# Kernel tuning notes

Measured on AMD Instinct MI355X. Metric: run time of the kernel, lower is better.

The kernel has to match this reference:

```python
import jax, jax.numpy as jnp
import numpy as np
from jax import lax

B, N, S, K = 16, 4096, 1024, 32
RADIUS = 0.2
C_IN = 64
BN_EPS = 1e-5


def setup_inputs() -> dict:
    key = jax.random.key(0)
    ks = jax.random.split(key, 6)
    x = jax.random.normal(ks[0], (B, N, 3), dtype=jnp.float32)
    x_complete = jax.random.normal(ks[1], (B, N, C_IN), dtype=jnp.float32)
    W0 = jax.random.normal(ks[2], (64, 67), dtype=jnp.float32) * 0.1
    W1 = jax.random.normal(ks[3], (64, 64), dtype=jnp.float32) * 0.1
    W2 = jax.random.normal(ks[4], (128, 64), dtype=jnp.float32) * 0.1
    return {
        "x": x, "x_complete": x_complete,
        "W0": W0, "b0": jnp.zeros(64), "g0": jnp.ones(64), "be0": jnp.zeros(64),
        "W1": W1, "b1": jnp.zeros(64), "g1": jnp.ones(64), "be1": jnp.zeros(64),
        "W2": W2, "b2": jnp.zeros(128), "g2": jnp.ones(128), "be2": jnp.zeros(128),
    }


def _fps(xyz, n_samples):
    """Farthest point sampling. xyz: [B,N,3] -> indices [B,n_samples] (int32)."""
    b, n, _ = xyz.shape
    batch_ar = jnp.arange(b)

    def step(carry, _):
        dists, farthest = carry                      # [B,N], [B]
        centroid = xyz[batch_ar, farthest]           # [B,3]
        d = jnp.sum((xyz - centroid[:, None, :]) ** 2, axis=-1)  # [B,N]
        dists = jnp.minimum(dists, d)
        nxt = jnp.argmax(dists, axis=-1).astype(jnp.int32)
        return (dists, nxt), farthest

    init = (jnp.full((b, n), 1e10, dtype=xyz.dtype), jnp.zeros(b, dtype=jnp.int32))
    _, idx = lax.scan(step, init, None, length=n_samples)
    return idx.T                                     # [B,n_samples]


def _ball_query(xyz, new_xyz, radius, k):
    """First-k points within radius of each centroid. Returns [B,S,K] int32."""
    b, n, _ = xyz.shape
    # squared distances centroid->point: [B,S,N]
    d2 = jnp.sum((new_xyz[:, :, None, :] - xyz[:, None, :, :]) ** 2, axis=-1)
    idx = jnp.where(d2 <= radius * radius, jnp.arange(n, dtype=jnp.int32), jnp.int32(n))
    idx = jnp.sort(idx, axis=-1)[..., :k]            # first k in index order
    first = idx[..., :1]                             # centroid itself is always in ball
    idx = jnp.where(idx == n, first, idx)
    return jnp.minimum(idx, n - 1)


def _gather_points(pts, idx_flat):
    """pts [B,N,C], idx_flat [B,M] -> [B,M,C]."""
    return jnp.take_along_axis(pts, idx_flat[..., None], axis=1)


def _conv_bn_relu(f, W, b, g, be):
    """f [B,C,M]; 1x1 Conv1d + training-mode BatchNorm1d + ReLU."""
    y = jnp.einsum('bcm,dc->bdm', f, W) + b[None, :, None]
    mu = jnp.mean(y, axis=(0, 2), keepdims=True)
    var = jnp.var(y, axis=(0, 2), keepdims=True)
    y = (y - mu) * lax.rsqrt(var + BN_EPS) * g[None, :, None] + be[None, :, None]
    return jax.nn.relu(y)


def reference(x, x_complete, W0, b0, g0, be0, W1, b1, g1, be1, W2, b2, g2, be2):
    # 1) FPS sampling of S centroids
    fps_idx = _fps(x, S)                                     # [B,S]
    new_xyz = _gather_points(x, fps_idx)                     # [B,S,3]
    # 2) Ball-query grouping of K neighbors per centroid
    idx = _ball_query(x, new_xyz, RADIUS, K)                 # [B,S,K]
    idx_flat = idx.reshape(B, S * K)
    grouped_xyz = _gather_points(x, idx_flat).reshape(B, S, K, 3)
    grouped_xyz = grouped_xyz - new_xyz[:, :, None, :]       # relative coords
    grouped_feat = _gather_points(x_complete, idx_flat).reshape(B, S, K, C_IN)
    f = jnp.concatenate([grouped_xyz, grouped_feat], axis=-1)  # [B,S,K,67]
    # 3) Shared MLP over channel dim (Conv1d k=1 + BN + ReLU), channels-first
    f = f.reshape(B, S * K, 3 + C_IN).transpose(0, 2, 1)     # [B,67,S*K]
    f = _conv_bn_relu(f, W0, b0, g0, be0)
    f = _conv_bn_relu(f, W1, b1, g1, be1)
    f = _conv_bn_relu(f, W2, b2, g2, be2)                    # [B,128,S*K]
    # 4) Max-pool over the K neighbors per centroid
    out = jnp.max(f.reshape(B, 128, S, K), axis=3)           # [B,128,S]
    return out
```

## Files before the change

### kernel.cpp

```cpp
#include <hip/hip_runtime.h>

namespace {
constexpr int kB = 16;
constexpr int kN = 4096;
constexpr int kS = 1024;
constexpr int kK = 32;
constexpr int kCF = 67;
constexpr int kSK = kS * kK;
constexpr int kPT = kB * kSK;
constexpr float kM = 524288.0f;

constexpr size_t kOffIdx   = 196608;
constexpr size_t kOffStats = 2293760;
constexpr size_t kOffScsh  = 2295808;
constexpr size_t kOffU     = 2297856;
constexpr size_t kWsNeedU  = kOffU + (size_t)kB * kN * 64 * sizeof(float);
constexpr size_t kOffPmax  = 19075072;
constexpr size_t kOffPmin  = kOffPmax + 8388608;
constexpr size_t kOffY1    = kOffPmin + 8388608;
constexpr size_t kWsNeedF  = kOffY1 + (size_t)kPT * 64 * 2;

constexpr int kLdsK = 72;

using bf16x8 = __attribute__((ext_vector_type(8))) short;
using f32x4  = __attribute__((ext_vector_type(4))) float;
}

__device__ __forceinline__ unsigned short f2bf(float f) {
  unsigned u = __float_as_uint(f);
  u += 0x7fffu + ((u >> 16) & 1u);
  return (unsigned short)(u >> 16);
}
__device__ __forceinline__ unsigned pack2bf(float a, float b) {
  return (unsigned)f2bf(a) | ((unsigned)f2bf(b) << 16);
}

template <int CTRL, int RM>
__device__ __forceinline__ float fmax_dpp(float x) {
  const int m = __builtin_amdgcn_update_dpp(__float_as_int(x), __float_as_int(x),
                                            CTRL, RM, 0xf, false);
  return fmaxf(x, __int_as_float(m));
}
template <int CTRL, int RM>
__device__ __forceinline__ unsigned umin_dpp(unsigned x) {
  const unsigned m = (unsigned)__builtin_amdgcn_update_dpp((int)x, (int)x,
                                                           CTRL, RM, 0xf, false);
  return x < m ? x : m;
}

__device__ void fps_body(const float* __restrict__ x, float* __restrict__ new_xyz,
                         int b, int tid, char* smem) {
  float* xs = (float*)smem;
  float* ys = xs + kN;
  float* zs = ys + kN;
  float* pv = zs + kN;
  int*   pi = (int*)(pv + 8);
  const int lane = tid & 63;
  const int wid = tid >> 6;
  const float* xb = x + (size_t)b * kN * 3;
  for (int q = tid; q < kN; q += 256) {
    xs[q] = xb[q * 3 + 0];
    ys[q] = xb[q * 3 + 1];
    zs[q] = xb[q * 3 + 2];
  }
  __syncthreads();
  float px[16], py[16], pz[16], dm[16];
#pragma unroll
  for (int j = 0; j < 16; ++j) {
    const int p = tid * 16 + j;
    px[j] = xs[p]; py[j] = ys[p]; pz[j] = zs[p];
    dm[j] = 1e10f;
  }
  int far = 0;
  for (int i = 0; i < kS; ++i) {
    const float cx = xs[far], cy = ys[far], cz = zs[far];
    if (tid == 0) {
      float* o = new_xyz + ((size_t)b * kS + i) * 3;
      o[0] = cx; o[1] = cy; o[2] = cz;
    }
#pragma unroll
    for (int j = 0; j < 16; ++j) {
      const float dx = __fsub_rn(px[j], cx);
      const float dy = __fsub_rn(py[j], cy);
      const float dz = __fsub_rn(pz[j], cz);
      const float t = __fadd_rn(__fadd_rn(__fmul_rn(dx, dx), __fmul_rn(dy, dy)),
                                __fmul_rn(dz, dz));
      dm[j] = fminf(dm[j], t);
    }
    const float m0 = fmaxf(fmaxf(dm[0], dm[1]), dm[2]);
    const float m1 = fmaxf(fmaxf(dm[3], dm[4]), dm[5]);
    const float m2 = fmaxf(fmaxf(dm[6], dm[7]), dm[8]);
    const float m3 = fmaxf(fmaxf(dm[9], dm[10]), dm[11]);
    const float m4 = fmaxf(fmaxf(dm[12], dm[13]), dm[14]);
    const float n0 = fmaxf(fmaxf(m0, m1), dm[15]);
    const float n1 = fmaxf(fmaxf(m2, m3), m4);
    float v = fmaxf(n0, n1);
    v = fmax_dpp<0x111, 0xf>(v);
    v = fmax_dpp<0x112, 0xf>(v);
    v = fmax_dpp<0x114, 0xf>(v);
    v = fmax_dpp<0x118, 0xf>(v);
    v = fmax_dpp<0x142, 0xa>(v);
    v = fmax_dpp<0x143, 0xc>(v);
    const float wv = __int_as_float(__builtin_amdgcn_readlane(__float_as_int(v), 63));
    unsigned msk = 0;
#pragma unroll
    for (int j = 0; j < 16; ++j) msk |= (dm[j] == wv ? 1u : 0u) << j;
    unsigned cand = msk ? ((unsigned)(tid * 16) + (unsigned)__builtin_ctz(msk))
                        : 0xffffffffu;
    cand = umin_dpp<0x111, 0xf>(cand);
    cand = umin_dpp<0x112, 0xf>(cand);
    cand = umin_dpp<0x114, 0xf>(cand);
    cand = umin_dpp<0x118, 0xf>(cand);
    cand = umin_dpp<0x142, 0xa>(cand);
    cand = umin_dpp<0x143, 0xc>(cand);
    const unsigned widx = (unsigned)__builtin_amdgcn_readlane((int)cand, 63);
    const int par = i & 1;
    if (lane == 0) { pv[par * 4 + wid] = wv; pi[par * 4 + wid] = (int)widx; }
    __syncthreads();
    float fv = pv[par * 4 + 0];
    int fi = pi[par * 4 + 0];
#pragma unroll
    for (int w = 1; w < 4; ++w) {
      const float v2 = pv[par * 4 + w];
      const int i2 = pi[par * 4 + w];
      if (v2 > fv) { fv = v2; fi = i2; }
    }
    far = fi;
  }
}

__device__ void u_body(const float* __restrict__ xc, const float* __restrict__ W0,
                       float* __restrict__ U, int ublk, int tid, char* smem) {
  unsigned short* a_lds = (unsigned short*)smem;
  unsigned short* w_lds = (unsigned short*)(smem + 128 * kLdsK * 2);
  const int r0 = ublk * 128;
  {
    const int pt = tid >> 1, half = tid & 1;
    const float4* src = (const float4*)(xc + ((size_t)(r0 + pt)) * 64 + half * 32);
    unsigned* dst = (unsigned*)(a_lds + pt * kLdsK + half * 32);
#pragma unroll
    for (int i = 0; i < 8; ++i) {
      const float4 v = src[i];
      dst[2 * i + 0] = pack2bf(v.x, v.y);
      dst[2 * i + 1] = pack2bf(v.z, v.w);
    }
  }
  for (int e = tid; e < 64 * 64; e += 256) {
    const int d = e >> 6, k2 = e & 63;
    w_lds[d * kLdsK + k2] = f2bf(W0[d * kCF + 3 + k2]);
  }
  __syncthreads();
  const int w = tid >> 6, lane = tid & 63, lr = lane & 15, lk = lane >> 4;
  f32x4 acc[2][4];
#pragma unroll
  for (int mi = 0; mi < 2; ++mi)
#pragma unroll
    for (int ni = 0; ni < 4; ++ni) acc[mi][ni] = (f32x4){0.f, 0.f, 0.f, 0.f};
#pragma unroll
  for (int ks = 0; ks < 2; ++ks) {
    const int k = lk * 8 + ks * 32;
    const bf16x8 a0 = *(const bf16x8*)(a_lds + (32 * w + lr) * kLdsK + k);
    const bf16x8 a1 = *(const bf16x8*)(a_lds + (32 * w + 16 + lr) * kLdsK + k);
#pragma unroll
    for (int ni = 0; ni < 4; ++ni) {
      const bf16x8 bv = *(const bf16x8*)(w_lds + (16 * ni + lr) * kLdsK + k);
      acc[0][ni] = __builtin_amdgcn_mfma_f32_16x16x32_bf16(a0, bv, acc[0][ni], 0, 0, 0);
      acc[1][ni] = __builtin_amdgcn_mfma_f32_16x16x32_bf16(a1, bv, acc[1][ni], 0, 0, 0);
    }
  }
#pragma unroll
  for (int mi = 0; mi < 2; ++mi)
#pragma unroll
    for (int ni = 0; ni < 4; ++ni)
#pragma unroll
      for (int r = 0; r < 4; ++r) {
        const int row = 32 * w + 16 * mi + lk * 4 + r;
        U[((size_t)(r0 + row)) * 64 + 16 * ni + lr] = acc[mi][ni][r];
      }
}

__global__ __launch_bounds__(256) void k1_kernel(const float* __restrict__ x,
                                                 const float* __restrict__ xc,
                                                 const float* __restrict__ W0,
                                                 float* __restrict__ nxyz,
                                                 float* __restrict__ U) {
  __shared__ __align__(16) char smem[49664];
  if (blockIdx.x < 16) fps_body(x, nxyz, blockIdx.x, threadIdx.x, smem);
  else u_body(xc, W0, U, blockIdx.x - 16, threadIdx.x, smem);
}

__global__ __launch_bounds__(256) void ballq_kernel(const float* __restrict__ x,
                                                    const float* __restrict__ new_xyz,
                                                    int* __restrict__ idx) {
  const int g = blockIdx.x * 4 + (threadIdx.x >> 6);
  const int lane = threadIdx.x & 63;
  const int b = g >> 10;
  const float* xb = x + (size_t)b * kN * 3;
  const float nx = new_xyz[g * 3 + 0];
  const float ny = new_xyz[g * 3 + 1];
  const float nz = new_xyz[g * 3 + 2];
  const float RR = (float)(0.2 * 0.2);
  int cnt = 0;
  int first = -1;
  for (int c = 0; c < kN / 64 && cnt < kK; ++c) {
    const int p = c * 64 + lane;
    const float dx = __fsub_rn(xb[p * 3 + 0], nx);
    const float dy = __fsub_rn(xb[p * 3 + 1], ny);
    const float dz = __fsub_rn(xb[p * 3 + 2], nz);
    const float t = __fadd_rn(__fadd_rn(__fmul_rn(dx, dx), __fmul_rn(dy, dy)),
                              __fmul_rn(dz, dz));
    const bool within = (t <= RR);
    const unsigned long long m = __ballot(within);
    if (first < 0 && m != 0ull) first = c * 64 + __builtin_ctzll(m);
    const int pos = cnt + (int)__popcll(m & ((1ull << lane) - 1ull));
    if (within && pos < kK) idx[(size_t)g * kK + pos] = p;
    cnt += (int)__popcll(m);
  }
  for (int k2 = cnt + lane; k2 < kK; k2 += 64) idx[(size_t)g * kK + k2] = first;
}

__global__ __launch_bounds__(256) void stats0_kernel(
    const float* __restrict__ x, const float* __restrict__ nxyz,
    const int* __restrict__ idx, const float* __restrict__ U,
    const float* __restrict__ W0, const float* __restrict__ b0,
    float* __restrict__ stats) {
  __shared__ float4 w0c[64];
  __shared__ float red[128];
  const int tid = threadIdx.x;
  if (tid < 64) w0c[tid] = make_float4(W0[tid * kCF + 0], W0[tid * kCF + 1],
                                       W0[tid * kCF + 2], b0[tid]);
  if (tid < 128) red[tid] = 0.0f;
  __syncthreads();
  const int gid = blockIdx.x * 256 + tid;
  const int half = gid & 1;
  const int pbase = gid >> 1;
  float s[32], q[32];
#pragma unroll
  for (int i = 0; i < 32; ++i) { s[i] = 0.f; q[i] = 0.f; }
  for (int r = 0; r < 8; ++r) {
    const int pt = pbase + r * 65536;
    const int v = idx[pt];
    const int b = pt >> 15;
    const int sc = (pt & (kSK - 1)) >> 5;
    const float* xp = x + ((size_t)b * kN + v) * 3;
    const float* np = nxyz + ((size_t)b * kS + sc) * 3;
    const float rx = xp[0] - np[0], ry = xp[1] - np[1], rz = xp[2] - np[2];
    const float4* up = (const float4*)(U + ((size_t)b * kN + v) * 64 + half * 32);
#pragma unroll
    for (int i = 0; i < 8; ++i) {
      const float4 u4 = up[i];
      const float uu[4] = {u4.x, u4.y, u4.z, u4.w};
#pragma unroll
      for (int j = 0; j < 4; ++j) {
        const float4 wc = w0c[half * 32 + i * 4 + j];
        const float y = uu[j] + rx * wc.x + ry * wc.y + rz * wc.z + wc.w;
        s[i * 4 + j] += y;
        q[i * 4 + j] += y * y;
      }
    }
  }
#pragma unroll
  for (int i = 0; i < 32; ++i) {
    const int c = half * 32 + i;
    atomicAdd(&red[c], s[i]);
    atomicAdd(&red[64 + c], q[i]);
  }
  __syncthreads();
  if (tid < 128) atomicAdd(&stats[tid], red[tid]);
}

__global__ void finalize_kernel(const float* __restrict__ g, const float* __restrict__ be,
                                const float* __restrict__ st, float* __restrict__ sc,
                                float* __restrict__ sh, int C) {
  const int c = threadIdx.x;
  if (c < C) {
    const float mean = st[c] / kM;
    const float var = st[C + c] / kM - mean * mean;
    const float scale = g[c] / sqrtf(var + 1e-5f);
    sc[c] = scale;
    sh[c] = be[c] - mean * scale;
  }
}

__global__ __launch_bounds__(256) void mlpA_kernel(
    const float* __restrict__ x, const float* __restrict__ nxyz,
    const int* __restrict__ idx, const float* __restrict__ U,
    const float* __restrict__ W0, const float* __restrict__ b0,
    const float* __restrict__ W1, const float* __restrict__ b1v,
    const float* __restrict__ scsh, float* __restrict__ stats,
    unsigned short* __restrict__ y1out) {
  __shared__ unsigned short a_lds[128 * kLdsK];
  __shared__ unsigned short w_lds[64 * kLdsK];
  __shared__ float red[128];
  __shared__ float4 w0c[64];
  __shared__ float2 sc0l[64];
  const int tid = threadIdx.x;
  const int p0 = blockIdx.x * 128;
  if (tid < 128) red[tid] = 0.0f;
  if (tid < 64) {
    w0c[tid] = make_float4(W0[tid * kCF + 0], W0[tid * kCF + 1],
                           W0[tid * kCF + 2], b0[tid]);
    sc0l[tid] = make_float2(scsh[tid], scsh[64 + tid]);
  }
  for (int f = tid; f < 64 * 16; f += 256) {
    const int d = f >> 4, k4 = (f & 15) * 4;
    const float4 vw = *(const float4*)(W1 + d * 64 + k4);
    unsigned* dst = (unsigned*)(w_lds + d * kLdsK + k4);
    dst[0] = pack2bf(vw.x, vw.y);
    dst[1] = pack2bf(vw.z, vw.w);
  }
  __syncthreads();
  {
    const int pt = tid >> 1, half = tid & 1;
    const int pg = p0 + pt;
    const int v = idx[pg];
    const int b = pg >> 15;
    const int sct = (pg & (kSK - 1)) >> 5;
    const float* xp = x + ((size_t)b * kN + v) * 3;
    const float* np = nxyz + ((size_t)b * kS + sct) * 3;
    const float rx = xp[0] - np[0], ry = xp[1] - np[1], rz = xp[2] - np[2];
    const float4* up = (const float4*)(U + ((size_t)b * kN + v) * 64 + half * 32);
    unsigned* dst = (unsigned*)(a_lds + pt * kLdsK + half * 32);
#pragma unroll
    for (int i = 0; i < 8; ++i) {
      const float4 u4 = up[i];
      const float uu[4] = {u4.x, u4.y, u4.z, u4.w};
      float a1[4];
#pragma unroll
      for (int j = 0; j < 4; ++j) {
        const int c = half * 32 + i * 4 + j;
        const float4 wc = w0c[c];
        const float y = uu[j] + rx * wc.x + ry * wc.y + rz * wc.z + wc.w;
        const float2 ss = sc0l[c];
        a1[j] = fmaxf(fmaf(y, ss.x, ss.y), 0.0f);
      }
      dst[2 * i + 0] = pack2bf(a1[0], a1[1]);
      dst[2 * i + 1] = pack2bf(a1[2], a1[3]);
    }
  }
  __syncthreads();

  const int w = tid >> 6, lane = tid & 63, lr = lane & 15, lk = lane >> 4;
  f32x4 acc1[2][4];
#pragma unroll
  for (int mi = 0; mi < 2; ++mi)
#pragma unroll
    for (int ni = 0; ni < 4; ++ni) acc1[mi][ni] = (f32x4){0.f, 0.f, 0.f, 0.f};
#pragma unroll
  for (int ks = 0; ks < 2; ++ks) {
    const int k = lk * 8 + ks * 32;
    const bf16x8 a0 = *(const bf16x8*)(a_lds + (32 * w + lr) * kLdsK + k);
    const bf16x8 a1 = *(const bf16x8*)(a_lds + (32 * w + 16 + lr) * kLdsK + k);
#pragma unroll
    for (int ni = 0; ni < 4; ++ni) {
      const bf16x8 bv = *(const bf16x8*)(w_lds + (16 * ni + lr) * kLdsK + k);
      acc1[0][ni] = __builtin_amdgcn_mfma_f32_16x16x32_bf16(a0, bv, acc1[0][ni], 0, 0, 0);
      acc1[1][ni] = __builtin_amdgcn_mfma_f32_16x16x32_bf16(a1, bv, acc1[1][ni], 0, 0, 0);
    }
  }
#pragma unroll
  for (int ni = 0; ni < 4; ++ni) {
    const int ch = 16 * ni + lr;
    const float bb = b1v[ch];
    float ss = 0.f, qq = 0.f;
#pragma unroll
    for (int mi = 0; mi < 2; ++mi)
#pragma unroll
      for (int r = 0; r < 4; ++r) {
        const float y = acc1[mi][ni][r] + bb;
        ss += y;
        qq += y * y;
        const int row = 32 * w + 16 * mi + lk * 4 + r;
        a_lds[row * kLdsK + ch] = f2bf(y);
      }
    atomicAdd(&red[ch], ss);
    atomicAdd(&red[64 + ch], qq);
  }
  __syncthreads();
  {
    const int row = tid >> 1, hf = tid & 1;
    const uint4* s4 = (const uint4*)(a_lds + row * kLdsK + hf * 32);
    uint4* d4 = (uint4*)(y1out + (size_t)(p0 + row) * 64 + hf * 32);
    d4[0] = s4[0]; d4[1] = s4[1]; d4[2] = s4[2]; d4[3] = s4[3];
  }
  if (tid < 128) atomicAdd(&stats[128 + tid], red[tid]);
}

__global__ __launch_bounds__(256) void mlpB_kernel(
    const unsigned short* __restrict__ y1in, const float* __restrict__ W2,
    const float* __restrict__ b2v, const float* __restrict__ scsh,
    float* __restrict__ stats, float* __restrict__ pmax,
    float* __restrict__ pmin) {
  __shared__ unsigned short a_lds[128 * kLdsK];
  __shared__ unsigned short w_lds[128 * kLdsK];
  __shared__ float red[256];
  __shared__ float2 s1l[64];
  const int tid = threadIdx.x;
  const int p0 = blockIdx.x * 128;
  red[tid] = 0.0f;
  if (tid < 64) s1l[tid] = make_float2(scsh[128 + tid], scsh[192 + tid]);
  __syncthreads();
  for (int f = tid; f < 128 * 16; f += 256) {
    const int d = f >> 4, k4 = (f & 15) * 4;
    const float4 vw = *(const float4*)(W2 + d * 64 + k4);
    unsigned* dst = (unsigned*)(w_lds + d * kLdsK + k4);
    dst[0] = pack2bf(vw.x, vw.y);
    dst[1] = pack2bf(vw.z, vw.w);
  }
  {
    const int row = tid >> 1, hf = tid & 1;
    const uint4* src = (const uint4*)(y1in + (size_t)(p0 + row) * 64 + hf * 32);
    const uint4 qa = src[0], qb = src[1], qc = src[2], qd = src[3];
    const unsigned in[16] = {qa.x, qa.y, qa.z, qa.w, qb.x, qb.y, qb.z, qb.w,
                             qc.x, qc.y, qc.z, qc.w, qd.x, qd.y, qd.z, qd.w};
    unsigned* dst = (unsigned*)(a_lds + row * kLdsK) + hf * 16;
#pragma unroll
    for (int i2 = 0; i2 < 16; ++i2) {
      const unsigned u = in[i2];
      const int ch0 = hf * 32 + i2 * 2;
      const float2 sA = s1l[ch0];
      const float2 sB = s1l[ch0 + 1];
      const float flo = __uint_as_float(u << 16);
      const float fhi = __uint_as_float(u & 0xffff0000u);
      const float alo = fmaxf(fmaf(flo, sA.x, sA.y), 0.0f);
      const float ahi = fmaxf(fmaf(fhi, sB.x, sB.y), 0.0f);
      dst[i2] = pack2bf(alo, ahi);
    }
  }
  __syncthreads();

  const int w = tid >> 6, lane = tid & 63, lr = lane & 15, lk = lane >> 4;
  f32x4 acc2[2][8];
#pragma unroll
  for (int mi = 0; mi < 2; ++mi)
#pragma unroll
    for (int ni = 0; ni < 8; ++ni) acc2[mi][ni] = (f32x4){0.f, 0.f, 0.f, 0.f};
#pragma unroll
  for (int ks = 0; ks < 2; ++ks) {
    const int k = lk * 8 + ks * 32;
    const bf16x8 a0 = *(const bf16x8*)(a_lds + (32 * w + lr) * kLdsK + k);
    const bf16x8 a1 = *(const bf16x8*)(a_lds + (32 * w + 16 + lr) * kLdsK + k);
#pragma unroll
    for (int ni = 0; ni < 8; ++ni) {
      const bf16x8 bv = *(const bf16x8*)(w_lds + (16 * ni + lr) * kLdsK + k);
      acc2[0][ni] = __builtin_amdgcn_mfma_f32_16x16x32_bf16(a0, bv, acc2[0][ni], 0, 0, 0);
      acc2[1][ni] = __builtin_amdgcn_mfma_f32_16x16x32_bf16(a1, bv, acc2[1][ni], 0, 0, 0);
    }
  }
  float mxv[8], mnv[8];
#pragma unroll
  for (int ni = 0; ni < 8; ++ni) {
    const int ch = 16 * ni + lr;
    const float bb = b2v[ch];
    float ss = 0.f, qq = 0.f;
    float mx = -3.4e38f, mn = 3.4e38f;
#pragma unroll
    for (int mi = 0; mi < 2; ++mi)
#pragma unroll
      for (int r = 0; r < 4; ++r) {
        const float a = acc2[mi][ni][r];
        const float y = a + bb;
        ss += y;
        qq += y * y;
        mx = fmaxf(mx, a);
        mn = fminf(mn, a);
      }
    atomicAdd(&red[ch], ss);
    atomicAdd(&red[128 + ch], qq);
    mx = fmaxf(mx, __shfl_xor(mx, 16, 64));
    mx = fmaxf(mx, __shfl_xor(mx, 32, 64));
    mn = fminf(mn, __shfl_xor(mn, 16, 64));
    mn = fminf(mn, __shfl_xor(mn, 32, 64));
    mxv[ni] = mx + bb;
    mnv[ni] = mn + bb;
  }
  __syncthreads();
  atomicAdd(&stats[256 + tid], red[tid]);
  const int pg0 = p0 + 32 * w;
  const int ob = pg0 >> 15;
  const int os = (pg0 & (kSK - 1)) >> 5;
  if (lane < 16) {
#pragma unroll
    for (int ni = 0; ni < 8; ++ni) {
      const size_t off = ((size_t)ob * 128 + 16 * ni + lane) * kS + os;
      pmax[off] = mxv[ni];
      pmin[off] = mnv[ni];
    }
  }
}

__global__ __launch_bounds__(256) void poolbn_kernel(
    const float* __restrict__ pmax, const float* __restrict__ pmin,
    const float* __restrict__ scsh, float* __restrict__ out) {
  const int gid = blockIdx.x * 256 + threadIdx.x;
  const int c = (gid >> 10) & 127;
  const float sc = scsh[256 + c];
  const float sh = scsh[384 + c];
  const float p = (sc >= 0.f) ? pmax[gid] : pmin[gid];
  out[gid] = fmaxf(fmaf(p, sc, sh), 0.0f);
}

template <int STAGE>
__global__ __launch_bounds__(256) void mlp_kernel(
    const float* __restrict__ x, const float* __restrict__ nxyz,
    const int* __restrict__ idx, const float* __restrict__ U,
    const float* __restrict__ W0, const float* __restrict__ b0,
    const float* __restrict__ W1, const float* __restrict__ b1v,
    const float* __restrict__ W2, const float* __restrict__ b2v,
    const float* __restrict__ scsh, float* __restrict__ stats,
    float* __restrict__ out) {
  __shared__ unsigned short a_lds[128 * kLdsK];
  __shared__ unsigned short w_lds[128 * kLdsK];
  __shared__ float red[256];
  __shared__ float4 w0c[64];
  __shared__ float2 sc0l[64];
  const int tid = threadIdx.x;
  const int p0 = blockIdx.x * 128;
  red[tid] = 0.0f;
  if (tid < 64) {
    w0c[tid] = make_float4(W0[tid * kCF + 0], W0[tid * kCF + 1],
                           W0[tid * kCF + 2], b0[tid]);
    sc0l[tid] = make_float2(scsh[tid], scsh[64 + tid]);
  }
  for (int f = tid; f < 64 * 16; f += 256) {
    const int d = f >> 4, k4 = (f & 15) * 4;
    const float4 vw = *(const float4*)(W1 + d * 64 + k4);
    unsigned* dst = (unsigned*)(w_lds + d * kLdsK + k4);
    dst[0] = pack2bf(vw.x, vw.y);
    dst[1] = pack2bf(vw.z, vw.w);
  }
  __syncthreads();
  {
    const int pt = tid >> 1, half = tid & 1;
    const int pg = p0 + pt;
    const int v = idx[pg];
    const int b = pg >> 15;
    const int sct = (pg & (kSK - 1)) >> 5;
    const float* xp = x + ((size_t)b * kN + v) * 3;
    const float* np = nxyz + ((size_t)b * kS + sct) * 3;
    const float rx = xp[0] - np[0], ry = xp[1] - np[1], rz = xp[2] - np[2];
    const float4* up = (const float4*)(U + ((size_t)b * kN + v) * 64 + half * 32);
    unsigned* dst = (unsigned*)(a_lds + pt * kLdsK + half * 32);
#pragma unroll
    for (int i = 0; i < 8; ++i) {
      const float4 u4 = up[i];
      const float uu[4] = {u4.x, u4.y, u4.z, u4.w};
      float a1[4];
#pragma unroll
      for (int j = 0; j < 4; ++j) {
        const int c = half * 32 + i * 4 + j;
        const float4 wc = w0c[c];
        const float y = uu[j] + rx * wc.x + ry * wc.y + rz * wc.z + wc.w;
        const float2 ss = sc0l[c];
        a1[j] = fmaxf(fmaf(y, ss.x, ss.y), 0.0f);
      }
      dst[2 * i + 0] = pack2bf(a1[0], a1[1]);
      dst[2 * i + 1] = pack2bf(a1[2], a1[3]);
    }
  }
  __syncthreads();

  const int w = tid >> 6, lane = tid & 63, lr = lane & 15, lk = lane >> 4;
  f32x4 acc1[2][4];
#pragma unroll
  for (int mi = 0; mi < 2; ++mi)
#pragma unroll
    for (int ni = 0; ni < 4; ++ni) acc1[mi][ni] = (f32x4){0.f, 0.f, 0.f, 0.f};
#pragma unroll
  for (int ks = 0; ks < 2; ++ks) {
    const int k = lk * 8 + ks * 32;
    const bf16x8 a0 = *(const bf16x8*)(a_lds + (32 * w + lr) * kLdsK + k);
    const bf16x8 a1 = *(const bf16x8*)(a_lds + (32 * w + 16 + lr) * kLdsK + k);
#pragma unroll
    for (int ni = 0; ni < 4; ++ni) {
      const bf16x8 bv = *(const bf16x8*)(w_lds + (16 * ni + lr) * kLdsK + k);
      acc1[0][ni] = __builtin_amdgcn_mfma_f32_16x16x32_bf16(a0, bv, acc1[0][ni], 0, 0, 0);
      acc1[1][ni] = __builtin_amdgcn_mfma_f32_16x16x32_bf16(a1, bv, acc1[1][ni], 0, 0, 0);
    }
  }

  if constexpr (STAGE == 1) {
#pragma unroll
    for (int ni = 0; ni < 4; ++ni) {
      const int ch = 16 * ni + lr;
      const float bb = b1v[ch];
      float ss = 0.f, qq = 0.f;
#pragma unroll
      for (int mi = 0; mi < 2; ++mi)
#pragma unroll
        for (int r = 0; r < 4; ++r) {
          const float y = acc1[mi][ni][r] + bb;
          ss += y;
          qq += y * y;
        }
      atomicAdd(&red[ch], ss);
      atomicAdd(&red[64 + ch], qq);
    }
    __syncthreads();
    if (tid < 128) atomicAdd(&stats[128 + tid], red[tid]);
    return;
  } else {
    __syncthreads();
#pragma unroll
    for (int ni = 0; ni < 4; ++ni) {
      const int ch = 16 * ni + lr;
      const float bb = b1v[ch];
      const float sc1 = scsh[128 + ch], sh1 = scsh[192 + ch];
#pragma unroll
      for (int mi = 0; mi < 2; ++mi)
#pragma unroll
        for (int r = 0; r < 4; ++r) {
          const int row = 32 * w + 16 * mi + lk * 4 + r;
          const float val = fmaxf(fmaf(acc1[mi][ni][r] + bb, sc1, sh1), 0.0f);
          a_lds[row * kLdsK + ch] = f2bf(val);
        }
    }
    for (int f = tid; f < 128 * 16; f += 256) {
      const int d = f >> 4, k4 = (f & 15) * 4;
      const float4 vw = *(const float4*)(W2 + d * 64 + k4);
      unsigned* dst = (unsigned*)(w_lds + d * kLdsK + k4);
      dst[0] = pack2bf(vw.x, vw.y);
      dst[1] = pack2bf(vw.z, vw.w);
    }
    __syncthreads();

    f32x4 acc2[2][8];
#pragma unroll
    for (int mi = 0; mi < 2; ++mi)
#pragma unroll
      for (int ni = 0; ni < 8; ++ni) acc2[mi][ni] = (f32x4){0.f, 0.f, 0.f, 0.f};
#pragma unroll
    for (int ks = 0; ks < 2; ++ks) {
      const int k = lk * 8 + ks * 32;
      const bf16x8 a0 = *(const bf16x8*)(a_lds + (32 * w + lr) * kLdsK + k);
      const bf16x8 a1 = *(const bf16x8*)(a_lds + (32 * w + 16 + lr) * kLdsK + k);
#pragma unroll
      for (int ni = 0; ni < 8; ++ni) {
        const bf16x8 bv = *(const bf16x8*)(w_lds + (16 * ni + lr) * kLdsK + k);
        acc2[0][ni] = __builtin_amdgcn_mfma_f32_16x16x32_bf16(a0, bv, acc2[0][ni], 0, 0, 0);
        acc2[1][ni] = __builtin_amdgcn_mfma_f32_16x16x32_bf16(a1, bv, acc2[1][ni], 0, 0, 0);
      }
    }

    if constexpr (STAGE == 2) {
#pragma unroll
      for (int ni = 0; ni < 8; ++ni) {
        const int ch = 16 * ni + lr;
        const float bb = b2v[ch];
        float ss = 0.f, qq = 0.f;
#pragma unroll
        for (int mi = 0; mi < 2; ++mi)
#pragma unroll
          for (int r = 0; r < 4; ++r) {
            const float y = acc2[mi][ni][r] + bb;
            ss += y;
            qq += y * y;
          }
        atomicAdd(&red[ch], ss);
        atomicAdd(&red[128 + ch], qq);
      }
      __syncthreads();
      atomicAdd(&stats[256 + tid], red[tid]);
    } else {
      float mx[8];
#pragma unroll
      for (int ni = 0; ni < 8; ++ni) {
        const int ch = 16 * ni + lr;
        const float bb = b2v[ch];
        const float sc2 = scsh[256 + ch], sh2 = scsh[384 + ch];
        float m = -1.0f;
#pragma unroll
        for (int mi = 0; mi < 2; ++mi)
#pragma unroll
          for (int r = 0; r < 4; ++r)
            m = fmaxf(m, fmaxf(fmaf(acc2[mi][ni][r] + bb, sc2, sh2), 0.0f));
        mx[ni] = m;
      }
#pragma unroll
      for (int ni = 0; ni < 8; ++ni) {
        mx[ni] = fmaxf(mx[ni], __shfl_xor(mx[ni], 16, 64));
        mx[ni] = fmaxf(mx[ni], __shfl_xor(mx[ni], 32, 64));
      }
      const int pg0 = p0 + 32 * w;
      const int ob = pg0 >> 15;
      const int os = (pg0 & (kSK - 1)) >> 5;
      if (lane < 16) {
#pragma unroll
        for (int ni = 0; ni < 8; ++ni)
          out[((size_t)ob * 128 + 16 * ni + lane) * kS + os] = mx[ni];
      }
    }
  }
}

extern "C" void kernel_launch(void* const* d_in, const int* in_sizes, int n_in,
                              void* d_out, int out_size, void* d_ws, size_t ws_size,
                              hipStream_t stream) {
  const float* x   = (const float*)d_in[0];
  const float* xc  = (const float*)d_in[1];
  const float* W0  = (const float*)d_in[2];
  const float* b0  = (const float*)d_in[3];
  const float* g0  = (const float*)d_in[4];
  const float* be0 = (const float*)d_in[5];
  const float* W1  = (const float*)d_in[6];
  const float* b1  = (const float*)d_in[7];
  const float* g1  = (const float*)d_in[8];
  const float* be1 = (const float*)d_in[9];
  const float* W2  = (const float*)d_in[10];
  const float* b2  = (const float*)d_in[11];
  const float* g2  = (const float*)d_in[12];
  const float* be2 = (const float*)d_in[13];
  float* out = (float*)d_out;
  char* ws = (char*)d_ws;
  float* nxyz  = (float*)(ws);
  int*   idx   = (int*)(ws + kOffIdx);
  float* stats = (float*)(ws + kOffStats);
  float* scsh  = (float*)(ws + kOffScsh);
  float* U     = (float*)(ws + kOffU);
  float* pmax  = (float*)(ws + kOffPmax);
  float* pmin  = (float*)(ws + kOffPmin);
  unsigned short* y1 = (unsigned short*)(ws + kOffY1);
  (void)in_sizes; (void)n_in; (void)out_size;

  hipMemsetAsync(stats, 0, 512 * sizeof(float), stream);
  k1_kernel<<<16 + 512, 256, 0, stream>>>(x, xc, W0, nxyz, U);
  ballq_kernel<<<(kB * kS) / 4, 256, 0, stream>>>(x, nxyz, idx);
  stats0_kernel<<<512, 256, 0, stream>>>(x, nxyz, idx, U, W0, b0, stats);
  finalize_kernel<<<1, 128, 0, stream>>>(g0, be0, stats, scsh, scsh + 64, 64);

  if (ws_size >= kWsNeedF) {
    mlpA_kernel<<<kPT / 128, 256, 0, stream>>>(x, nxyz, idx, U, W0, b0, W1, b1,
                                               scsh, stats, y1);
    finalize_kernel<<<1, 128, 0, stream>>>(g1, be1, stats + 128, scsh + 128, scsh + 192, 64);
    mlpB_kernel<<<kPT / 128, 256, 0, stream>>>(y1, W2, b2, scsh, stats, pmax, pmin);
    finalize_kernel<<<1, 128, 0, stream>>>(g2, be2, stats + 256, scsh + 256, scsh + 384, 128);
    poolbn_kernel<<<(kB * 128 * kS) / 256, 256, 0, stream>>>(pmax, pmin, scsh, out);
  } else {
    mlp_kernel<1><<<kPT / 128, 256, 0, stream>>>(x, nxyz, idx, U, W0, b0, W1, b1,
                                                 W2, b2, scsh, stats, out);
    finalize_kernel<<<1, 128, 0, stream>>>(g1, be1, stats + 128, scsh + 128, scsh + 192, 64);
    mlp_kernel<2><<<kPT / 128, 256, 0, stream>>>(x, nxyz, idx, U, W0, b0, W1, b1,
                                                 W2, b2, scsh, stats, out);
    finalize_kernel<<<1, 128, 0, stream>>>(g2, be2, stats + 256, scsh + 256, scsh + 384, 128);
    mlp_kernel<3><<<kPT / 128, 256, 0, stream>>>(x, nxyz, idx, U, W0, b0, W1, b1,
                                                 W2, b2, scsh, stats, out);
  }
}
```

Measured before the change: 1.187 ms.

## Overlap ball query and BN0 stats with FPS using in-kernel progress flags

Fuses the ball-query and layer-0 statistics kernels into the FPS/U kernel as persistent worker blocks. The workers spin on per-batch progress flags that FPS publishes every 16 centroids, plus a counter for U completion, so neighbour search overlaps the long serial FPS loop instead of waiting for it. The FPS argmax is also reworked to pack distance and inverted index into a 64-bit key, giving a single max reduction instead of a max pass followed by an index-min pass. The FPS blocks get raised wave priority. This relies on all blocks being co-resident, since spin-waiting blocks could deadlock if the producer blocks are not scheduled, and the sleeping waiters take CU slots alongside the FPS waves.

```diff
diff --git a/kernel.cpp b/kernel.cpp
--- a/kernel.cpp
+++ b/kernel.cpp
@@ -13,9 +13,9 @@
 constexpr size_t kOffIdx   = 196608;
 constexpr size_t kOffStats = 2293760;
 constexpr size_t kOffScsh  = 2295808;
-constexpr size_t kOffU     = 2297856;
-constexpr size_t kWsNeedU  = kOffU + (size_t)kB * kN * 64 * sizeof(float);
-constexpr size_t kOffPmax  = 19075072;
+constexpr size_t kOffFlags = 2297856;
+constexpr size_t kOffU     = 2297984;
+constexpr size_t kOffPmax  = kOffU + 16777216;
 constexpr size_t kOffPmin  = kOffPmax + 8388608;
 constexpr size_t kOffY1    = kOffPmin + 8388608;
 constexpr size_t kWsNeedF  = kOffY1 + (size_t)kPT * 64 * 2;
@@ -24,6 +24,7 @@
 
 using bf16x8 = __attribute__((ext_vector_type(8))) short;
 using f32x4  = __attribute__((ext_vector_type(4))) float;
+using u64 = unsigned long long;
 }
 
 __device__ __forceinline__ unsigned short f2bf(float f) {
@@ -35,26 +36,24 @@
   return (unsigned)f2bf(a) | ((unsigned)f2bf(b) << 16);
 }
 
+__device__ __forceinline__ u64 kmax(u64 a, u64 b) { return a > b ? a : b; }
+
 template <int CTRL, int RM>
-__device__ __forceinline__ float fmax_dpp(float x) {
-  const int m = __builtin_amdgcn_update_dpp(__float_as_int(x), __float_as_int(x),
-                                            CTRL, RM, 0xf, false);
-  return fmaxf(x, __int_as_float(m));
-}
-template <int CTRL, int RM>
-__device__ __forceinline__ unsigned umin_dpp(unsigned x) {
-  const unsigned m = (unsigned)__builtin_amdgcn_update_dpp((int)x, (int)x,
-                                                           CTRL, RM, 0xf, false);
-  return x < m ? x : m;
+__device__ __forceinline__ u64 kmax_dpp(u64 x) {
+  const unsigned hi = (unsigned)(x >> 32), lo = (unsigned)x;
+  const unsigned h2 = (unsigned)__builtin_amdgcn_update_dpp((int)hi, (int)hi, CTRL, RM, 0xf, false);
+  const unsigned l2 = (unsigned)__builtin_amdgcn_update_dpp((int)lo, (int)lo, CTRL, RM, 0xf, false);
+  const u64 y = ((u64)h2 << 32) | l2;
+  return x > y ? x : y;
 }
 
 __device__ void fps_body(const float* __restrict__ x, float* __restrict__ new_xyz,
-                         int b, int tid, char* smem) {
+                         int* __restrict__ flags, int b, int tid, char* smem) {
+  __builtin_amdgcn_s_setprio(3);
   float* xs = (float*)smem;
   float* ys = xs + kN;
   float* zs = ys + kN;
-  float* pv = zs + kN;
-  int*   pi = (int*)(pv + 8);
+  u64* pvu = (u64*)(smem + 49152);
   const int lane = tid & 63;
   const int wid = tid >> 6;
   const float* xb = x + (size_t)b * kN * 3;
@@ -65,11 +64,13 @@
   }
   __syncthreads();
   float px[16], py[16], pz[16], dm[16];
+  unsigned invc[16];
 #pragma unroll
   for (int j = 0; j < 16; ++j) {
     const int p = tid * 16 + j;
     px[j] = xs[p]; py[j] = ys[p]; pz[j] = zs[p];
     dm[j] = 1e10f;
+    invc[j] = 0xffffffffu - (unsigned)p;
   }
   int far = 0;
   for (int i = 0; i < kS; ++i) {
@@ -77,6 +78,9 @@
     if (tid == 0) {
       float* o = new_xyz + ((size_t)b * kS + i) * 3;
       o[0] = cx; o[1] = cy; o[2] = cz;
+      if ((i & 15) == 15)
+        __hip_atomic_store(&flags[b], i + 1, __ATOMIC_RELEASE,
+                           __HIP_MEMORY_SCOPE_AGENT);
     }
 #pragma unroll
     for (int j = 0; j < 16; ++j) {
@@ -87,50 +91,36 @@
                                 __fmul_rn(dz, dz));
       dm[j] = fminf(dm[j], t);
     }
-    const float m0 = fmaxf(fmaxf(dm[0], dm[1]), dm[2]);
-    const float m1 = fmaxf(fmaxf(dm[3], dm[4]), dm[5]);
-    const float m2 = fmaxf(fmaxf(dm[6], dm[7]), dm[8]);
-    const float m3 = fmaxf(fmaxf(dm[9], dm[10]), dm[11]);
-    const float m4 = fmaxf(fmaxf(dm[12], dm[13]), dm[14]);
-    const float n0 = fmaxf(fmaxf(m0, m1), dm[15]);
-    const float n1 = fmaxf(fmaxf(m2, m3), m4);
-    float v = fmaxf(n0, n1);
-    v = fmax_dpp<0x111, 0xf>(v);
-    v = fmax_dpp<0x112, 0xf>(v);
-    v = fmax_dpp<0x114, 0xf>(v);
-    v = fmax_dpp<0x118, 0xf>(v);
-    v = fmax_dpp<0x142, 0xa>(v);
-    v = fmax_dpp<0x143, 0xc>(v);
-    const float wv = __int_as_float(__builtin_amdgcn_readlane(__float_as_int(v), 63));
-    unsigned msk = 0;
-#pragma unroll
-    for (int j = 0; j < 16; ++j) msk |= (dm[j] == wv ? 1u : 0u) << j;
-    unsigned cand = msk ? ((unsigned)(tid * 16) + (unsigned)__builtin_ctz(msk))
-                        : 0xffffffffu;
-    cand = umin_dpp<0x111, 0xf>(cand);
-    cand = umin_dpp<0x112, 0xf>(cand);
-    cand = umin_dpp<0x114, 0xf>(cand);
-    cand = umin_dpp<0x118, 0xf>(cand);
-    cand = umin_dpp<0x142, 0xa>(cand);
-    cand = umin_dpp<0x143, 0xc>(cand);
-    const unsigned widx = (unsigned)__builtin_amdgcn_readlane((int)cand, 63);
+    u64 k[16];
+#pragma unroll
+    for (int j = 0; j < 16; ++j)
+      k[j] = ((u64)__float_as_uint(dm[j]) << 32) | invc[j];
+    u64 t8[8], t4[4], t2[2];
+#pragma unroll
+    for (int j = 0; j < 8; ++j) t8[j] = kmax(k[j], k[j + 8]);
+#pragma unroll
+    for (int j = 0; j < 4; ++j) t4[j] = kmax(t8[j], t8[j + 4]);
+#pragma unroll
+    for (int j = 0; j < 2; ++j) t2[j] = kmax(t4[j], t4[j + 2]);
+    u64 v = kmax(t2[0], t2[1]);
+    v = kmax_dpp<0x111, 0xf>(v);
+    v = kmax_dpp<0x112, 0xf>(v);
+    v = kmax_dpp<0x114, 0xf>(v);
+    v = kmax_dpp<0x118, 0xf>(v);
+    v = kmax_dpp<0x142, 0xa>(v);
+    v = kmax_dpp<0x143, 0xc>(v);
     const int par = i & 1;
-    if (lane == 0) { pv[par * 4 + wid] = wv; pi[par * 4 + wid] = (int)widx; }
+    if (lane == 63) pvu[par * 4 + wid] = v;
     __syncthreads();
-    float fv = pv[par * 4 + 0];
-    int fi = pi[par * 4 + 0];
-#pragma unroll
-    for (int w = 1; w < 4; ++w) {
-      const float v2 = pv[par * 4 + w];
-      const int i2 = pi[par * 4 + w];
-      if (v2 > fv) { fv = v2; fi = i2; }
-    }
-    far = fi;
+    const u64 mm = kmax(kmax(pvu[par * 4 + 0], pvu[par * 4 + 1]),
+                        kmax(pvu[par * 4 + 2], pvu[par * 4 + 3]));
+    far = (int)(0xffffffffu - (unsigned)mm);
   }
 }
 
 __device__ void u_body(const float* __restrict__ xc, const float* __restrict__ W0,
-                       float* __restrict__ U, int ublk, int tid, char* smem) {
+                       float* __restrict__ U, int* __restrict__ flags,
+                       int ublk, int tid, char* smem) {
   unsigned short* a_lds = (unsigned short*)smem;
   unsigned short* w_lds = (unsigned short*)(smem + 128 * kLdsK * 2);
   const int r0 = ublk * 128;
@@ -177,74 +167,68 @@
         const int row = 32 * w + 16 * mi + lk * 4 + r;
         U[((size_t)(r0 + row)) * 64 + 16 * ni + lr] = acc[mi][ni][r];
       }
-}
-
-__global__ __launch_bounds__(256) void k1_kernel(const float* __restrict__ x,
-                                                 const float* __restrict__ xc,
-                                                 const float* __restrict__ W0,
-                                                 float* __restrict__ nxyz,
-                                                 float* __restrict__ U) {
-  __shared__ __align__(16) char smem[49664];
-  if (blockIdx.x < 16) fps_body(x, nxyz, blockIdx.x, threadIdx.x, smem);
-  else u_body(xc, W0, U, blockIdx.x - 16, threadIdx.x, smem);
-}
-
-__global__ __launch_bounds__(256) void ballq_kernel(const float* __restrict__ x,
-                                                    const float* __restrict__ new_xyz,
-                                                    int* __restrict__ idx) {
-  const int g = blockIdx.x * 4 + (threadIdx.x >> 6);
-  const int lane = threadIdx.x & 63;
-  const int b = g >> 10;
-  const float* xb = x + (size_t)b * kN * 3;
-  const float nx = new_xyz[g * 3 + 0];
-  const float ny = new_xyz[g * 3 + 1];
-  const float nz = new_xyz[g * 3 + 2];
-  const float RR = (float)(0.2 * 0.2);
-  int cnt = 0;
-  int first = -1;
-  for (int c = 0; c < kN / 64 && cnt < kK; ++c) {
-    const int p = c * 64 + lane;
-    const float dx = __fsub_rn(xb[p * 3 + 0], nx);
-    const float dy = __fsub_rn(xb[p * 3 + 1], ny);
-    const float dz = __fsub_rn(xb[p * 3 + 2], nz);
-    const float t = __fadd_rn(__fadd_rn(__fmul_rn(dx, dx), __fmul_rn(dy, dy)),
-                              __fmul_rn(dz, dz));
-    const bool within = (t <= RR);
-    const unsigned long long m = __ballot(within);
-    if (first < 0 && m != 0ull) first = c * 64 + __builtin_ctzll(m);
-    const int pos = cnt + (int)__popcll(m & ((1ull << lane) - 1ull));
-    if (within && pos < kK) idx[(size_t)g * kK + pos] = p;
-    cnt += (int)__popcll(m);
-  }
-  for (int k2 = cnt + lane; k2 < kK; k2 += 64) idx[(size_t)g * kK + k2] = first;
-}
-
-__global__ __launch_bounds__(256) void stats0_kernel(
-    const float* __restrict__ x, const float* __restrict__ nxyz,
-    const int* __restrict__ idx, const float* __restrict__ U,
-    const float* __restrict__ W0, const float* __restrict__ b0,
-    float* __restrict__ stats) {
-  __shared__ float4 w0c[64];
-  __shared__ float red[128];
-  const int tid = threadIdx.x;
+  __syncthreads();
+  if (tid == 0)
+    __hip_atomic_fetch_add(&flags[16], 1, __ATOMIC_RELEASE,
+                           __HIP_MEMORY_SCOPE_AGENT);
+}
+
+__device__ void ballq_stats_body(const float* __restrict__ x,
+                                 const float* __restrict__ nxyz,
+                                 int* __restrict__ idx,
+                                 const float* __restrict__ U,
+                                 const float* __restrict__ W0,
+                                 const float* __restrict__ b0,
+                                 float* __restrict__ stats,
+                                 int* __restrict__ flags,
+                                 int blk, int tid, char* smem) {
+  float* red = (float*)smem;
+  float4* w0c = (float4*)(smem + 512);
+  if (tid < 128) red[tid] = 0.0f;
   if (tid < 64) w0c[tid] = make_float4(W0[tid * kCF + 0], W0[tid * kCF + 1],
                                        W0[tid * kCF + 2], b0[tid]);
-  if (tid < 128) red[tid] = 0.0f;
-  __syncthreads();
-  const int gid = blockIdx.x * 256 + tid;
-  const int half = gid & 1;
-  const int pbase = gid >> 1;
-  float s[32], q[32];
-#pragma unroll
-  for (int i = 0; i < 32; ++i) { s[i] = 0.f; q[i] = 0.f; }
-  for (int r = 0; r < 8; ++r) {
-    const int pt = pbase + r * 65536;
-    const int v = idx[pt];
-    const int b = pt >> 15;
-    const int sc = (pt & (kSK - 1)) >> 5;
+  __syncthreads();
+  const int wid = tid >> 6, lane = tid & 63;
+  const int W = blk * 4 + wid;
+  while (__hip_atomic_load(&flags[16], __ATOMIC_RELAXED,
+                           __HIP_MEMORY_SCOPE_AGENT) < 512)
+    __builtin_amdgcn_s_sleep(32);
+  (void)__hip_atomic_load(&flags[16], __ATOMIC_ACQUIRE, __HIP_MEMORY_SCOPE_AGENT);
+  const float RR = (float)(0.2 * 0.2);
+  const int half = lane & 1;
+  float s_acc[32], q_acc[32];
+#pragma unroll
+  for (int i = 0; i < 32; ++i) { s_acc[i] = 0.f; q_acc[i] = 0.f; }
+  for (int g = W; g < kB * kS; g += 896) {
+    const int b = g >> 10;
+    const int s = g & 1023;
+    while (__hip_atomic_load(&flags[b], __ATOMIC_RELAXED,
+                             __HIP_MEMORY_SCOPE_AGENT) <= s)
+      __builtin_amdgcn_s_sleep(32);
+    (void)__hip_atomic_load(&flags[b], __ATOMIC_ACQUIRE, __HIP_MEMORY_SCOPE_AGENT);
+    const float nx = nxyz[g * 3 + 0];
+    const float ny = nxyz[g * 3 + 1];
+    const float nz = nxyz[g * 3 + 2];
+    const float* xb = x + (size_t)b * kN * 3;
+    int cnt = 0, first = -1;
+    for (int c = 0; c < kN / 64 && cnt < kK; ++c) {
+      const int p = c * 64 + lane;
+      const float dx = __fsub_rn(xb[p * 3 + 0], nx);
+      const float dy = __fsub_rn(xb[p * 3 + 1], ny);
+      const float dz = __fsub_rn(xb[p * 3 + 2], nz);
+      const float t = __fadd_rn(__fadd_rn(__fmul_rn(dx, dx), __fmul_rn(dy, dy)),
+                                __fmul_rn(dz, dz));
+      const bool within = (t <= RR);
+      const unsigned long long m = __ballot(within);
+      if (first < 0 && m != 0ull) first = c * 64 + __builtin_ctzll(m);
+      const int pos = cnt + (int)__popcll(m & ((1ull << lane) - 1ull));
+      if (within && pos < kK) idx[(size_t)g * kK + pos] = p;
+      cnt += (int)__popcll(m);
+    }
+    for (int k2 = cnt + lane; k2 < kK; k2 += 64) idx[(size_t)g * kK + k2] = first;
+    const int v = idx[(size_t)g * kK + (lane >> 1)];
     const float* xp = x + ((size_t)b * kN + v) * 3;
-    const float* np = nxyz + ((size_t)b * kS + sc) * 3;
-    const float rx = xp[0] - np[0], ry = xp[1] - np[1], rz = xp[2] - np[2];
+    const float rx = xp[0] - nx, ry = xp[1] - ny, rz = xp[2] - nz;
     const float4* up = (const float4*)(U + ((size_t)b * kN + v) * 64 + half * 32);
 #pragma unroll
     for (int i = 0; i < 8; ++i) {
@@ -254,19 +238,33 @@
       for (int j = 0; j < 4; ++j) {
         const float4 wc = w0c[half * 32 + i * 4 + j];
         const float y = uu[j] + rx * wc.x + ry * wc.y + rz * wc.z + wc.w;
-        s[i * 4 + j] += y;
-        q[i * 4 + j] += y * y;
+        s_acc[i * 4 + j] += y;
+        q_acc[i * 4 + j] += y * y;
       }
     }
   }
 #pragma unroll
   for (int i = 0; i < 32; ++i) {
-    const int c = half * 32 + i;
-    atomicAdd(&red[c], s[i]);
-    atomicAdd(&red[64 + c], q[i]);
+    atomicAdd(&red[half * 32 + i], s_acc[i]);
+    atomicAdd(&red[64 + half * 32 + i], q_acc[i]);
   }
   __syncthreads();
   if (tid < 128) atomicAdd(&stats[tid], red[tid]);
+}
+
+__global__ __launch_bounds__(256, 3) void k1_kernel(
+    const float* __restrict__ x, const float* __restrict__ xc,
+    const float* __restrict__ W0, const float* __restrict__ b0,
+    float* __restrict__ nxyz, float* __restrict__ U, int* __restrict__ idx,
+    float* __restrict__ stats, int* __restrict__ flags) {
+  __shared__ __align__(16) char smem[49664];
+  if (blockIdx.x < 16)
+    fps_body(x, nxyz, flags, blockIdx.x, threadIdx.x, smem);
+  else if (blockIdx.x < 528)
+    u_body(xc, W0, U, flags, blockIdx.x - 16, threadIdx.x, smem);
+  else
+    ballq_stats_body(x, nxyz, idx, U, W0, b0, stats, flags,
+                     blockIdx.x - 528, threadIdx.x, smem);
 }
 
 __global__ void finalize_kernel(const float* __restrict__ g, const float* __restrict__ be,
@@ -716,16 +714,16 @@
   int*   idx   = (int*)(ws + kOffIdx);
   float* stats = (float*)(ws + kOffStats);
   float* scsh  = (float*)(ws + kOffScsh);
+  int*   flags = (int*)(ws + kOffFlags);
   float* U     = (float*)(ws + kOffU);
   float* pmax  = (float*)(ws + kOffPmax);
   float* pmin  = (float*)(ws + kOffPmin);
   unsigned short* y1 = (unsigned short*)(ws + kOffY1);
   (void)in_sizes; (void)n_in; (void)out_size;
 
-  hipMemsetAsync(stats, 0, 512 * sizeof(float), stream);
-  k1_kernel<<<16 + 512, 256, 0, stream>>>(x, xc, W0, nxyz, U);
-  ballq_kernel<<<(kB * kS) / 4, 256, 0, stream>>>(x, nxyz, idx);
-  stats0_kernel<<<512, 256, 0, stream>>>(x, nxyz, idx, U, W0, b0, stats);
+  hipMemsetAsync(stats, 0, 4224, stream);
+  k1_kernel<<<16 + 512 + 224, 256, 0, stream>>>(x, xc, W0, b0, nxyz, U, idx,
+                                                stats, flags);
   finalize_kernel<<<1, 128, 0, stream>>>(g0, be0, stats, scsh, scsh + 64, 64);
 
   if (ws_size >= kWsNeedF) {
```

After: 1.381 ms. +16.3%, slower.
